# Kernel optimization log

Hardware: AMD Instinct MI355X
Metric: run time of the kernel (lower is better)

Reference implementation:

```python
import jax, jax.numpy as jnp
import numpy as np

B, NV, NRINGS, NDIRS, NF = 4, 50000, 3, 16, 16


def setup_inputs() -> dict:
    key = jax.random.key(0)
    k1, k2, k3, k4 = jax.random.split(key, 4)
    basepoints = jax.random.normal(k1, (B, NV, 3), dtype=jnp.float32)
    local_frames = jax.random.normal(k2, (B, NV, 3, 3), dtype=jnp.float32)
    # expmap: gather_nd indices into basepoints' (batch, vertex) dims
    vidx = jax.random.randint(k3, (B, NV, NRINGS, NDIRS), 0, NV, dtype=jnp.int32)
    bidx = jnp.broadcast_to(jnp.arange(B, dtype=jnp.int32)[:, None, None, None],
                            (B, NV, NRINGS, NDIRS))
    expmap = jnp.stack([bidx, vidx], axis=-1)  # (B, NV, NRINGS, NDIRS, 2)
    kernel = jax.random.normal(k4, (NRINGS, NDIRS, 3, NF), dtype=jnp.float32) * 0.05
    bias = jnp.zeros((NF,), dtype=jnp.float32)
    return {"basepoints": basepoints, "local_frames": local_frames,
            "expmap": expmap, "kernel": kernel, "bias": bias}


def reference(basepoints, local_frames, expmap, kernel, bias):
    b, nv = basepoints.shape[0], basepoints.shape[1]
    nrings, ndirs = expmap.shape[2], expmap.shape[3]
    nf = kernel.shape[-1]
    # gather_nd: neighbor coordinates per (ring, direction)
    y = basepoints[expmap[..., 0], expmap[..., 1]]          # (b, nv, nrings, ndirs, 3)
    # center at basepoint
    y = y - basepoints[:, :, None, None, :]
    # rotate into local frame
    y = jnp.einsum('bvkl,bvrdl->bvrdk', local_frames, y)    # (b, nv, nrings, ndirs, 3)
    # patch conv with ring wraparound (circular padding along direction axis)
    y = y.reshape(b * nv, nrings, ndirs, 3)
    y = jnp.concatenate([y, y[:, :, :-1, :]], axis=2)       # (b*nv, nrings, 2*ndirs-1, 3)
    y = jax.lax.conv_general_dilated(
        y, kernel, window_strides=(1, 1), padding='VALID',
        dimension_numbers=('NHWC', 'HWIO', 'NHWC'))         # (b*nv, 1, ndirs, nf)
    y = y.reshape(b, nv, ndirs, nf) + bias
    return jax.nn.relu(y)
```

## Files before the change

### kernel.cpp

```cpp
#include <hip/hip_runtime.h>
#include <hip/hip_bf16.h>

#define NBATCH 4
#define NV     50000
#define VPB    4
#define VST    304
#define CP1    295

typedef __attribute__((ext_vector_type(8))) short short8;
typedef __attribute__((ext_vector_type(4))) float floatx4;

__global__ void build_wfrag(const float* __restrict__ kw,
                            unsigned short* __restrict__ wbuf) {
    const int lane = threadIdx.x;
    const int fcol = lane & 15;
    const int quad = lane >> 4;
    #pragma unroll
    for (int kc = 0; kc < 5; ++kc) {
        unsigned short v[8];
        #pragma unroll
        for (int j = 0; j < 8; ++j) {
            int k = kc * 32 + quad * 8 + j;
            unsigned short b = 0;
            if (k < 144) {
                int dd = k / 9;
                int q  = k - dd * 9;
                int r  = q / 3;
                int c  = q - r * 3;
                __hip_bfloat16 h = __float2bfloat16(kw[((r * 16 + dd) * 3 + c) * 16 + fcol]);
                __builtin_memcpy(&b, &h, 2);
            }
            v[j] = b;
        }
        __builtin_memcpy(wbuf + lane * 40 + kc * 8, v, 16);
    }
}

__global__ __launch_bounds__(64, 8)
void input3d_mfma(const float* __restrict__ bp,
                  const float* __restrict__ fr,
                  const int2*  __restrict__ em,
                  const unsigned short* __restrict__ wbuf,
                  const float* __restrict__ bias,
                  float*       __restrict__ out)
{
    __shared__ __align__(16) unsigned short yls[VPB * 2 * VST];

    const int tid  = threadIdx.x;
    const int bv0  = blockIdx.x * VPB;
    const int lane = tid;
    const int fcol = lane & 15;
    const int quad = lane >> 4;

    union WU { unsigned short s[8]; short8 v; };
    WU wf[5];
    const unsigned short* wl = wbuf + lane * 40;
    #pragma unroll
    for (int kc = 0; kc < 5; ++kc)
        __builtin_memcpy(&wf[kc].s[0], wl + kc * 8, 16);
    const float bsf = bias[fcol];

    {
        const int v   = tid >> 4;
        const int dir = tid & 15;
        const int bv  = bv0 + v;
        float F[9];
        __builtin_memcpy(&F[0], fr + (size_t)bv * 9, 16);
        __builtin_memcpy(&F[4], fr + (size_t)bv * 9 + 4, 16);
        F[8] = fr[(size_t)bv * 9 + 8];
        const float c0 = bp[bv * 3 + 0];
        const float c1 = bp[bv * 3 + 1];
        const float c2 = bp[bv * 3 + 2];

        unsigned short val[9];
        #pragma unroll
        for (int r = 0; r < 3; ++r) {
            int2 e  = em[bv * 48 + r * 16 + dir];
            int nb  = e.x * NV + e.y;
            float dx = bp[nb * 3 + 0] - c0;
            float dy = bp[nb * 3 + 1] - c1;
            float dz = bp[nb * 3 + 2] - c2;
            #pragma unroll
            for (int c = 0; c < 3; ++c) {
                float yv = F[c * 3 + 0] * dx + F[c * 3 + 1] * dy + F[c * 3 + 2] * dz;
                __hip_bfloat16 h = __float2bfloat16(yv);
                unsigned short us;
                __builtin_memcpy(&us, &h, 2);
                val[r * 3 + c] = us;
            }
        }

        unsigned short* buf = &yls[v * 2 * VST];
        unsigned int pe[4], po[4];
        #pragma unroll
        for (int i = 0; i < 4; ++i) {
            pe[i] = (unsigned int)val[2 * i]     | ((unsigned int)val[2 * i + 1] << 16);
            po[i] = (unsigned int)val[2 * i + 1] | ((unsigned int)val[2 * i + 2] << 16);
        }
        const int n0 = dir * 9;
        auto storeE = [&](int s) {
            unsigned int* p = (unsigned int*)(buf + s);
            p[0] = pe[0]; p[1] = pe[1]; p[2] = pe[2]; p[3] = pe[3];
            buf[s + 8] = val[8];
        };
        auto storeO = [&](int s) {
            buf[s] = val[0];
            unsigned int* p = (unsigned int*)(buf + s + 1);
            p[0] = po[0]; p[1] = po[1]; p[2] = po[2]; p[3] = po[3];
        };
        if (dir & 1) {
            storeO(n0);
            storeE(CP1 + n0);
            if (dir < 15) { storeO(n0 + 144); storeE(CP1 + n0 + 144); }
        } else {
            storeE(n0);
            storeO(CP1 + n0);
            if (dir < 15) { storeE(n0 + 144); storeO(CP1 + n0 + 144); }
        }
    }
    __syncthreads();

    floatx4 acc[4] = {{0.f,0.f,0.f,0.f},{0.f,0.f,0.f,0.f},
                      {0.f,0.f,0.f,0.f},{0.f,0.f,0.f,0.f}};
    const unsigned short* abase[4];
    #pragma unroll
    for (int i = 0; i < 4; ++i) {
        abase[i] = &yls[i * 2 * VST + ((fcol & 1) ? CP1 : 0) + 9 * fcol];
    }
    #pragma unroll
    for (int kc = 0; kc < 4; ++kc) {
        const int s = kc * 32 + quad * 8;
        #pragma unroll
        for (int i = 0; i < 4; ++i) {
            const unsigned int* pa = (const unsigned int*)(abase[i] + s);
            union { unsigned int u[4]; short8 s8; } a;
            a.u[0] = pa[0]; a.u[1] = pa[1]; a.u[2] = pa[2]; a.u[3] = pa[3];
            acc[i] = __builtin_amdgcn_mfma_f32_16x16x32_bf16(a.s8, wf[kc].v, acc[i], 0, 0, 0);
        }
    }
    {
        const int s = 128 + quad * 8;
        #pragma unroll
        for (int i = 0; i < 4; ++i) {
            union { unsigned int u[4]; short8 s8; } a;
            if (quad < 2) {
                const unsigned int* pa = (const unsigned int*)(abase[i] + s);
                a.u[0] = pa[0]; a.u[1] = pa[1]; a.u[2] = pa[2]; a.u[3] = pa[3];
            } else {
                a.u[0] = 0; a.u[1] = 0; a.u[2] = 0; a.u[3] = 0;
            }
            acc[i] = __builtin_amdgcn_mfma_f32_16x16x32_bf16(a.s8, wf[4].v, acc[i], 0, 0, 0);
        }
    }

    #pragma unroll
    for (int i = 0; i < 4; ++i) {
        int vg = bv0 + i;
        float* ob = out + (size_t)vg * 256;
        #pragma unroll
        for (int rr = 0; rr < 4; ++rr) {
            float o = acc[i][rr] + bsf;
            o = o > 0.f ? o : 0.f;
            ob[(quad * 4 + rr) * 16 + fcol] = o;
        }
    }
}

extern "C" void kernel_launch(void* const* d_in, const int* in_sizes, int n_in,
                              void* d_out, int out_size, void* d_ws, size_t ws_size,
                              hipStream_t stream) {
    const float* bp   = (const float*)d_in[0];
    const float* fr   = (const float*)d_in[1];
    const int2*  em   = (const int2*)d_in[2];
    const float* kw   = (const float*)d_in[3];
    const float* bias = (const float*)d_in[4];
    float* out = (float*)d_out;
    unsigned short* wbuf = (unsigned short*)d_ws;

    build_wfrag<<<1, 64, 0, stream>>>(kw, wbuf);

    const int total_bv = NBATCH * NV;
    const int grid = total_bv / VPB;
    input3d_mfma<<<grid, 64, 0, stream>>>(bp, fr, em, wbuf, bias, out);
}
```

Baseline: 343.9 us.

## Split fused kernel into gather/rotate pass and MFMA matmul pass via workspace

```diff
diff --git a/kernel.cpp b/kernel.cpp
--- a/kernel.cpp
+++ b/kernel.cpp
@@ -3,9 +3,10 @@
 
 #define NBATCH 4
 #define NV     50000
-#define VPB    4
 #define VST    304
 #define CP1    295
+#define VPB2   8
+#define VPBF   4
 
 typedef __attribute__((ext_vector_type(8))) short short8;
 typedef __attribute__((ext_vector_type(4))) float floatx4;
@@ -36,18 +37,170 @@
     }
 }
 
+__device__ __forceinline__ void compute_val(const float* __restrict__ bp,
+                                            const float* __restrict__ fr,
+                                            const int2* __restrict__ em,
+                                            int bv, int dir,
+                                            unsigned short val[9]) {
+    float F[9];
+    __builtin_memcpy(&F[0], fr + (size_t)bv * 9, 16);
+    __builtin_memcpy(&F[4], fr + (size_t)bv * 9 + 4, 16);
+    F[8] = fr[(size_t)bv * 9 + 8];
+    const float c0 = bp[bv * 3 + 0];
+    const float c1 = bp[bv * 3 + 1];
+    const float c2 = bp[bv * 3 + 2];
+    #pragma unroll
+    for (int r = 0; r < 3; ++r) {
+        int2 e  = em[bv * 48 + r * 16 + dir];
+        int nb  = e.x * NV + e.y;
+        float dx = bp[nb * 3 + 0] - c0;
+        float dy = bp[nb * 3 + 1] - c1;
+        float dz = bp[nb * 3 + 2] - c2;
+        #pragma unroll
+        for (int c = 0; c < 3; ++c) {
+            float yv = F[c * 3 + 0] * dx + F[c * 3 + 1] * dy + F[c * 3 + 2] * dz;
+            __hip_bfloat16 h = __float2bfloat16(yv);
+            unsigned short us;
+            __builtin_memcpy(&us, &h, 2);
+            val[r * 3 + c] = us;
+        }
+    }
+}
+
+__global__ __launch_bounds__(256, 4)
+void gather_rot(const float* __restrict__ bp,
+                const float* __restrict__ fr,
+                const int2*  __restrict__ em,
+                unsigned short* __restrict__ yw) {
+    const int tid = threadIdx.x;
+    const int bv  = blockIdx.x * 16 + (tid >> 4);
+    const int dir = tid & 15;
+    unsigned short val[9];
+    compute_val(bp, fr, em, bv, dir, val);
+    unsigned int pe[4], po[4];
+    #pragma unroll
+    for (int i = 0; i < 4; ++i) {
+        pe[i] = (unsigned int)val[2 * i]     | ((unsigned int)val[2 * i + 1] << 16);
+        po[i] = (unsigned int)val[2 * i + 1] | ((unsigned int)val[2 * i + 2] << 16);
+    }
+    unsigned short* wv = yw + (size_t)bv * 144;
+    const int n0 = dir * 9;
+    if (dir & 1) {
+        wv[n0] = val[0];
+        unsigned int* p = (unsigned int*)(wv + n0 + 1);
+        p[0] = po[0]; p[1] = po[1]; p[2] = po[2]; p[3] = po[3];
+    } else {
+        unsigned int* p = (unsigned int*)(wv + n0);
+        p[0] = pe[0]; p[1] = pe[1]; p[2] = pe[2]; p[3] = pe[3];
+        wv[n0 + 8] = val[8];
+    }
+}
+
+__global__ __launch_bounds__(64, 4)
+void mm_store(const unsigned short* __restrict__ yw,
+              const unsigned short* __restrict__ wbuf,
+              const float* __restrict__ bias,
+              float*       __restrict__ out) {
+    __shared__ __align__(16) unsigned short yls[VPB2 * 2 * VST];
+
+    const int lane = threadIdx.x;
+    const int bv0  = blockIdx.x * VPB2;
+    const int fcol = lane & 15;
+    const int quad = lane >> 4;
+
+    union WU { unsigned short s[8]; short8 v; };
+    WU wf[5];
+    const unsigned short* wl = wbuf + lane * 40;
+    #pragma unroll
+    for (int kc = 0; kc < 5; ++kc)
+        __builtin_memcpy(&wf[kc].s[0], wl + kc * 8, 16);
+    const float bsf = bias[fcol];
+
+    unsigned int w9[9];
+    const unsigned int* src = (const unsigned int*)(yw + (size_t)bv0 * 144);
+    #pragma unroll
+    for (int j = 0; j < 9; ++j) w9[j] = src[lane + j * 64];
+
+    #pragma unroll
+    for (int j = 0; j < 9; ++j) {
+        const int p  = lane + j * 64;
+        const int v  = p / 72;
+        const int t  = (p - v * 72) * 2;
+        const int VB = v * 2 * VST;
+        const unsigned int w = w9[j];
+        const unsigned short lo = (unsigned short)w;
+        const unsigned short hi = (unsigned short)(w >> 16);
+        *(unsigned int*)&yls[VB + t] = w;
+        yls[VB + CP1 + t]     = lo;
+        yls[VB + CP1 + t + 1] = hi;
+        if (t <= 132) {
+            *(unsigned int*)&yls[VB + 144 + t] = w;
+            yls[VB + CP1 + 144 + t]     = lo;
+            yls[VB + CP1 + 144 + t + 1] = hi;
+        } else if (t == 134) {
+            yls[VB + 278]       = lo;
+            yls[VB + CP1 + 278] = lo;
+        }
+    }
+    __syncthreads();
+
+    floatx4 acc[VPB2];
+    #pragma unroll
+    for (int i = 0; i < VPB2; ++i) acc[i] = {0.f, 0.f, 0.f, 0.f};
+    const unsigned short* abase[VPB2];
+    #pragma unroll
+    for (int i = 0; i < VPB2; ++i)
+        abase[i] = &yls[i * 2 * VST + ((fcol & 1) ? CP1 : 0) + 9 * fcol];
+    #pragma unroll
+    for (int kc = 0; kc < 4; ++kc) {
+        const int s = kc * 32 + quad * 8;
+        #pragma unroll
+        for (int i = 0; i < VPB2; ++i) {
+            const unsigned int* pa = (const unsigned int*)(abase[i] + s);
+            union { unsigned int u[4]; short8 s8; } a;
+            a.u[0] = pa[0]; a.u[1] = pa[1]; a.u[2] = pa[2]; a.u[3] = pa[3];
+            acc[i] = __builtin_amdgcn_mfma_f32_16x16x32_bf16(a.s8, wf[kc].v, acc[i], 0, 0, 0);
+        }
+    }
+    {
+        const int s = 128 + quad * 8;
+        #pragma unroll
+        for (int i = 0; i < VPB2; ++i) {
+            union { unsigned int u[4]; short8 s8; } a;
+            if (quad < 2) {
+                const unsigned int* pa = (const unsigned int*)(abase[i] + s);
+                a.u[0] = pa[0]; a.u[1] = pa[1]; a.u[2] = pa[2]; a.u[3] = pa[3];
+            } else {
+                a.u[0] = 0; a.u[1] = 0; a.u[2] = 0; a.u[3] = 0;
+            }
+            acc[i] = __builtin_amdgcn_mfma_f32_16x16x32_bf16(a.s8, wf[4].v, acc[i], 0, 0, 0);
+        }
+    }
+
+    #pragma unroll
+    for (int i = 0; i < VPB2; ++i) {
+        int vg = bv0 + i;
+        float* ob = out + (size_t)vg * 256;
+        #pragma unroll
+        for (int rr = 0; rr < 4; ++rr) {
+            float o = acc[i][rr] + bsf;
+            o = o > 0.f ? o : 0.f;
+            ob[(quad * 4 + rr) * 16 + fcol] = o;
+        }
+    }
+}
+
 __global__ __launch_bounds__(64, 8)
 void input3d_mfma(const float* __restrict__ bp,
                   const float* __restrict__ fr,
                   const int2*  __restrict__ em,
                   const unsigned short* __restrict__ wbuf,
                   const float* __restrict__ bias,
-                  float*       __restrict__ out)
-{
-    __shared__ __align__(16) unsigned short yls[VPB * 2 * VST];
+                  float*       __restrict__ out) {
+    __shared__ __align__(16) unsigned short yls[VPBF * 2 * VST];
 
     const int tid  = threadIdx.x;
-    const int bv0  = blockIdx.x * VPB;
+    const int bv0  = blockIdx.x * VPBF;
     const int lane = tid;
     const int fcol = lane & 15;
     const int quad = lane >> 4;
@@ -63,33 +216,8 @@
     {
         const int v   = tid >> 4;
         const int dir = tid & 15;
-        const int bv  = bv0 + v;
-        float F[9];
-        __builtin_memcpy(&F[0], fr + (size_t)bv * 9, 16);
-        __builtin_memcpy(&F[4], fr + (size_t)bv * 9 + 4, 16);
-        F[8] = fr[(size_t)bv * 9 + 8];
-        const float c0 = bp[bv * 3 + 0];
-        const float c1 = bp[bv * 3 + 1];
-        const float c2 = bp[bv * 3 + 2];
-
         unsigned short val[9];
-        #pragma unroll
-        for (int r = 0; r < 3; ++r) {
-            int2 e  = em[bv * 48 + r * 16 + dir];
-            int nb  = e.x * NV + e.y;
-            float dx = bp[nb * 3 + 0] - c0;
-            float dy = bp[nb * 3 + 1] - c1;
-            float dz = bp[nb * 3 + 2] - c2;
-            #pragma unroll
-            for (int c = 0; c < 3; ++c) {
-                float yv = F[c * 3 + 0] * dx + F[c * 3 + 1] * dy + F[c * 3 + 2] * dz;
-                __hip_bfloat16 h = __float2bfloat16(yv);
-                unsigned short us;
-                __builtin_memcpy(&us, &h, 2);
-                val[r * 3 + c] = us;
-            }
-        }
-
+        compute_val(bp, fr, em, bv0 + v, dir, val);
         unsigned short* buf = &yls[v * 2 * VST];
         unsigned int pe[4], po[4];
         #pragma unroll
@@ -120,18 +248,17 @@
     }
     __syncthreads();
 
-    floatx4 acc[4] = {{0.f,0.f,0.f,0.f},{0.f,0.f,0.f,0.f},
-                      {0.f,0.f,0.f,0.f},{0.f,0.f,0.f,0.f}};
-    const unsigned short* abase[4];
-    #pragma unroll
-    for (int i = 0; i < 4; ++i) {
+    floatx4 acc[VPBF] = {{0.f,0.f,0.f,0.f},{0.f,0.f,0.f,0.f},
+                         {0.f,0.f,0.f,0.f},{0.f,0.f,0.f,0.f}};
+    const unsigned short* abase[VPBF];
+    #pragma unroll
+    for (int i = 0; i < VPBF; ++i)
         abase[i] = &yls[i * 2 * VST + ((fcol & 1) ? CP1 : 0) + 9 * fcol];
-    }
     #pragma unroll
     for (int kc = 0; kc < 4; ++kc) {
         const int s = kc * 32 + quad * 8;
         #pragma unroll
-        for (int i = 0; i < 4; ++i) {
+        for (int i = 0; i < VPBF; ++i) {
             const unsigned int* pa = (const unsigned int*)(abase[i] + s);
             union { unsigned int u[4]; short8 s8; } a;
             a.u[0] = pa[0]; a.u[1] = pa[1]; a.u[2] = pa[2]; a.u[3] = pa[3];
@@ -141,7 +268,7 @@
     {
         const int s = 128 + quad * 8;
         #pragma unroll
-        for (int i = 0; i < 4; ++i) {
+        for (int i = 0; i < VPBF; ++i) {
             union { unsigned int u[4]; short8 s8; } a;
             if (quad < 2) {
                 const unsigned int* pa = (const unsigned int*)(abase[i] + s);
@@ -152,9 +279,8 @@
             acc[i] = __builtin_amdgcn_mfma_f32_16x16x32_bf16(a.s8, wf[4].v, acc[i], 0, 0, 0);
         }
     }
-
-    #pragma unroll
-    for (int i = 0; i < 4; ++i) {
+    #pragma unroll
+    for (int i = 0; i < VPBF; ++i) {
         int vg = bv0 + i;
         float* ob = out + (size_t)vg * 256;
         #pragma unroll
@@ -180,6 +306,12 @@
     build_wfrag<<<1, 64, 0, stream>>>(kw, wbuf);
 
     const int total_bv = NBATCH * NV;
-    const int grid = total_bv / VPB;
-    input3d_mfma<<<grid, 64, 0, stream>>>(bp, fr, em, wbuf, bias, out);
-}
+    const size_t need = 8192 + (size_t)total_bv * 144 * 2;
+    if (ws_size >= need) {
+        unsigned short* yw = (unsigned short*)((char*)d_ws + 8192);
+        gather_rot<<<total_bv / 16, 256, 0, stream>>>(bp, fr, em, yw);
+        mm_store<<<total_bv / VPB2, 64, 0, stream>>>(yw, wbuf, bias, out);
+    } else {
+        input3d_mfma<<<total_bv / VPBF, 64, 0, stream>>>(bp, fr, em, wbuf, bias, out);
+    }
+}
```

Result: slower. 452.3 us (+31.5%).
